# Performance work log

Measured on AMD Instinct MI355X. Metric: run time of the kernel, lower is better.

Reference implementation:

```python
import jax, jax.numpy as jnp
import numpy as np

T, B, D, H = 512, 64, 512, 512  # seq_len, batch, input_size, hidden_size


def setup_inputs() -> dict:
    key = jax.random.key(0)
    ks = jax.random.split(key, 7)
    s = jnp.float32(0.05)  # keep gates out of saturation
    return {
        "x": jax.random.normal(ks[0], (T, B, D), jnp.float32),
        "Wi_l0": jax.random.normal(ks[1], (2, 4 * H, D), jnp.float32) * s,
        "Wh_l0": jax.random.normal(ks[2], (2, 4 * H, H), jnp.float32) * s,
        "b_l0": jax.random.normal(ks[3], (2, 4 * H), jnp.float32) * s,
        "Wi_l1": jax.random.normal(ks[4], (2, 4 * H, 2 * H), jnp.float32) * s,
        "Wh_l1": jax.random.normal(ks[5], (2, 4 * H, H), jnp.float32) * s,
        "b_l1": jax.random.normal(ks[6], (2, 4 * H), jnp.float32) * s,
    }


def _lstm_dir(xs, Wi, Wh, b):
    """Run one LSTM direction over xs: [T, B, Din] -> ([T, B, H], h_T, c_T)."""
    Bsz = xs.shape[1]
    Hh = Wh.shape[-1]
    # Precompute input contribution for all timesteps (the big GEMM).
    gx = jnp.einsum('tbd,gd->tbg', xs, Wi) + b  # [T, B, 4H]

    def step(carry, gx_t):
        h, c = carry
        gates = gx_t + h @ Wh.T  # [B, 4H]
        i, f, g, o = jnp.split(gates, 4, axis=-1)
        c = jax.nn.sigmoid(f) * c + jax.nn.sigmoid(i) * jnp.tanh(g)
        h = jax.nn.sigmoid(o) * jnp.tanh(c)
        return (h, c), h

    h0 = jnp.zeros((Bsz, Hh), xs.dtype)
    (hT, cT), hs = jax.lax.scan(step, (h0, h0), gx)
    return hs, hT, cT


def _bilstm_layer(xs, Wi, Wh, b):
    hf, hTf, cTf = _lstm_dir(xs, Wi[0], Wh[0], b[0])
    hb, hTb, cTb = _lstm_dir(xs[::-1], Wi[1], Wh[1], b[1])
    # torch.stack(dim=2).view(T, B, -1) == concat along feature axis
    out = jnp.concatenate([hf, hb[::-1]], axis=-1)  # [T, B, 2H]
    return out, (hTf, hTb), (cTf, cTb)


def reference(x, Wi_l0, Wh_l0, b_l0, Wi_l1, Wh_l1, b_l1):
    o0, h0s, c0s = _bilstm_layer(x, Wi_l0, Wh_l0, b_l0)
    o1, h1s, c1s = _bilstm_layer(o0, Wi_l1, Wh_l1, b_l1)
    # state order: (layer0 fwd, layer0 bwd, layer1 fwd, layer1 bwd)
    h_n = jnp.stack(h0s + h1s, axis=0)  # [4, B, H]
    c_n = jnp.stack(c0s + c1s, axis=0)  # [4, B, H]
    return o1, (h_n, c_n)
```

## Files before the change

kernel.cpp:

```cpp
#include <hip/hip_runtime.h>
#include <stdint.h>


#define TT 512
#define BATCH 64
#define HH 512
#define NWG 64
#define NCOLS 32

typedef __attribute__((ext_vector_type(8))) short vshort8;
typedef __attribute__((ext_vector_type(4))) float vfloat4;
typedef __attribute__((ext_vector_type(4))) unsigned int vuint4;

__device__ __forceinline__ vfloat4 mfma16(vshort8 a, vshort8 b, vfloat4 c) {
    return __builtin_amdgcn_mfma_f32_16x16x32_bf16(a, b, c, 0, 0, 0);
}

__device__ __forceinline__ float sigmoidf_(float x) {
    return 1.f / (1.f + __expf(-x));
}
__device__ __forceinline__ float tanhf_(float x) {
    float e = __expf(2.f * x);
    return 1.f - 2.f / (e + 1.f);
}
__device__ __forceinline__ unsigned short f2bf(float f) {
    uint32_t u = __float_as_uint(f);
    uint32_t r = (u + 0x7fffu + ((u >> 16) & 1u)) >> 16;
    return (unsigned short)r;
}

__global__ void cvt_f32_bf16(const float* __restrict__ src,
                             unsigned short* __restrict__ dst, int n) {
    int i = (blockIdx.x * blockDim.x + threadIdx.x) * 4;
    if (i + 3 < n) {
        float4 v = *(const float4*)(src + i);
        uint2 p;
        p.x = (uint32_t)f2bf(v.x) | ((uint32_t)f2bf(v.y) << 16);
        p.y = (uint32_t)f2bf(v.z) | ((uint32_t)f2bf(v.w) << 16);
        *(uint2*)(dst + i) = p;
    }
}

template <int DIN, bool WRITE_BF16>
__launch_bounds__(256, 1)
__global__ void lstm_phase(const unsigned short* __restrict__ A,
                           const unsigned short* __restrict__ Wi,
                           const float* __restrict__ Whf,
                           const float* __restrict__ bias,
                           uint32_t* __restrict__ hbuf32,
                           unsigned short* __restrict__ obf,
                           float* __restrict__ of32,
                           float* __restrict__ hn,
                           float* __restrict__ cn)
{
    __shared__ unsigned short Wlds[NCOLS * DIN];
    __shared__ unsigned short Whlds[NCOLS * HH];

    const int tid = threadIdx.x;
    const int dir = blockIdx.x >> 6;
    const int wg = blockIdx.x & 63;
    const int j0 = wg * 8;
    const int lane = tid & 63;
    const int wave = tid >> 6;

    for (int chunk = tid; chunk < NCOLS * DIN / 8; chunk += 256) {
        int n = chunk / (DIN / 8);
        int k8 = (chunk % (DIN / 8)) * 8;
        int grow = (n >> 3) * HH + j0 + (n & 7);
        vshort8 v = *(const vshort8*)(Wi + ((size_t)dir * 4 * HH + grow) * DIN + k8);
        int byte = n * DIN * 2 + ((k8 * 2) ^ ((n & 7) << 4));
        *(vshort8*)((char*)Wlds + byte) = v;
    }
    for (int chunk = tid; chunk < NCOLS * HH / 8; chunk += 256) {
        int n = chunk / (HH / 8);
        int k8 = (chunk % (HH / 8)) * 8;
        int grow = (n >> 3) * HH + j0 + (n & 7);
        const float* src = Whf + ((size_t)dir * 4 * HH + grow) * HH + k8;
        float4 f0 = *(const float4*)(src);
        float4 f1 = *(const float4*)(src + 4);
        vshort8 v;
        v[0] = (short)f2bf(f0.x); v[1] = (short)f2bf(f0.y);
        v[2] = (short)f2bf(f0.z); v[3] = (short)f2bf(f0.w);
        v[4] = (short)f2bf(f1.x); v[5] = (short)f2bf(f1.y);
        v[6] = (short)f2bf(f1.z); v[7] = (short)f2bf(f1.w);
        int byte = n * HH * 2 + ((k8 * 2) ^ ((n & 7) << 4));
        *(vshort8*)((char*)Whlds + byte) = v;
    }
    __syncthreads();

    const int arow = wave * 16 + (lane & 15);
    const int kOff = (lane >> 4) * 8;
    const int klane = (lane >> 4) * 16;
    const int n0 = lane & 15;
    const int swz = (n0 & 7) << 4;
    const int nb0 = n0 * DIN * 2;
    const int nb1 = (16 + n0) * DIN * 2;
    const int nb0h = n0 * HH * 2;
    const int nb1h = (16 + n0) * HH * 2;
    const int grow0 = (n0 >> 3) * HH + j0 + (n0 & 7);
    const int grow1 = ((n0 >> 3) + 2) * HH + j0 + (n0 & 7);
    const float bias0 = bias[dir * 4 * HH + grow0];
    const float bias1 = bias[dir * 4 * HH + grow1];
    const bool lo = (lane & 8) == 0;
    const int jcol = j0 + (lane & 7);
    const int hrowb = wave * 16 + ((lane >> 4) << 2);
    const int scol = (lane & 15) * 32 + (lane >> 4) * 8;

    float cstate[4] = {0.f, 0.f, 0.f, 0.f};

    for (int s = 0; s < TT; ++s) {
        const int t = dir ? (TT - 1 - s) : s;

        vfloat4 acc0, acc1;
        acc0[0] = acc0[1] = acc0[2] = acc0[3] = bias0;
        acc1[0] = acc1[1] = acc1[2] = acc1[3] = bias1;

        const unsigned short* ap = A + ((size_t)t * BATCH + arow) * DIN + kOff;
#pragma unroll 8
        for (int kk = 0; kk < DIN / 32; ++kk) {
            vshort8 a = *(const vshort8*)(ap + kk * 32);
            int kb = kk * 64 + klane;
            vshort8 b0 = *(const vshort8*)((const char*)Wlds + nb0 + (kb ^ swz));
            vshort8 b1 = *(const vshort8*)((const char*)Wlds + nb1 + (kb ^ swz));
            acc0 = mfma16(a, b0, acc0);
            acc1 = mfma16(a, b1, acc1);
        }

        if (s > 0) {
            const uint32_t* rowbase =
                hbuf32 + (((dir << 1) | ((s - 1) & 1)) * BATCH + arow) * HH;
            const uint32_t* rbase = rowbase + kOff;
            const uint32_t want = (uint32_t)s;

            for (;;) {
                uint32_t sent;
                asm volatile(
                    "global_load_dword %0, %1, off sc0 sc1\n\t"
                    "s_waitcnt vmcnt(0)"
                    : "=v"(sent) : "v"(rowbase + scol) : "memory");
                if (!__any(((sent ^ want) & 0xffffu) != 0)) break;
                __builtin_amdgcn_s_sleep(1);
            }

            vuint4 hd[32];
            for (;;) {
#pragma unroll
                for (int q = 0; q < 32; ++q)
                    asm volatile("global_load_dwordx4 %0, %1, off sc0 sc1"
                                 : "=v"(hd[q])
                                 : "v"(rbase + (q >> 1) * 32 + (q & 1) * 4));
                asm volatile("s_waitcnt vmcnt(0)" ::: "memory");
                __builtin_amdgcn_sched_barrier(0);
                uint32_t diff = 0;
#pragma unroll
                for (int q = 0; q < 32; ++q)
                    diff |= (hd[q][0] ^ want) | (hd[q][1] ^ want) |
                            (hd[q][2] ^ want) | (hd[q][3] ^ want);
                if (!__any((diff & 0xffffu) != 0)) break;
                __builtin_amdgcn_s_sleep(1);
            }
            __builtin_amdgcn_sched_barrier(0);

#pragma unroll
            for (int kk = 0; kk < 16; ++kk) {
                uint32_t d0 = __builtin_amdgcn_perm(hd[2 * kk][1], hd[2 * kk][0], 0x07060302u);
                uint32_t d1 = __builtin_amdgcn_perm(hd[2 * kk][3], hd[2 * kk][2], 0x07060302u);
                uint32_t d2 = __builtin_amdgcn_perm(hd[2 * kk + 1][1], hd[2 * kk + 1][0], 0x07060302u);
                uint32_t d3 = __builtin_amdgcn_perm(hd[2 * kk + 1][3], hd[2 * kk + 1][2], 0x07060302u);
                vuint4 tt = {d0, d1, d2, d3};
                vshort8 ha = __builtin_bit_cast(vshort8, tt);
                int kb = kk * 64 + klane;
                vshort8 b0 = *(const vshort8*)((const char*)Whlds + nb0h + (kb ^ swz));
                vshort8 b1 = *(const vshort8*)((const char*)Whlds + nb1h + (kb ^ swz));
                acc0 = mfma16(ha, b0, acc0);
                acc1 = mfma16(ha, b1, acc1);
            }
        }

        float hval[4];
#pragma unroll
        for (int r = 0; r < 4; ++r) {
            float own0 = acc0[r], own1 = acc1[r];
            float oth0 = __shfl_xor(own0, 8, 64);
            float oth1 = __shfl_xor(own1, 8, 64);
            float iv = lo ? own0 : oth0;
            float fv = lo ? oth0 : own0;
            float gv = lo ? own1 : oth1;
            float ov = lo ? oth1 : own1;
            float cnew = sigmoidf_(fv) * cstate[r] + sigmoidf_(iv) * tanhf_(gv);
            cstate[r] = cnew;
            hval[r] = sigmoidf_(ov) * tanhf_(cnew);
        }

        uint32_t* hw = hbuf32 + (size_t)(((dir << 1) | (s & 1)) * BATCH) * HH;
        const int rA = lo ? 0 : 2;
        const uint32_t tagv = (uint32_t)(s + 1);
#pragma unroll
        for (int q = 0; q < 2; ++q) {
            int r = rA + q, row = hrowb + r;
            unsigned short hb = f2bf(hval[r]);
            uint32_t val = ((uint32_t)hb << 16) | tagv;
            uint32_t* wp = hw + row * HH + jcol;
            asm volatile("global_store_dword %0, %1, off sc0 sc1"
                         :: "v"(wp), "v"(val) : "memory");
            if constexpr (WRITE_BF16)
                obf[((size_t)t * BATCH + row) * (2 * HH) + dir * HH + jcol] = hb;
            else
                of32[((size_t)t * BATCH + row) * (2 * HH) + dir * HH + jcol] = hval[r];
        }
        if (s == TT - 1) {
#pragma unroll
            for (int q = 0; q < 2; ++q) {
                int r = rA + q, row = hrowb + r;
                hn[(dir * BATCH + row) * HH + jcol] = hval[r];
                cn[(dir * BATCH + row) * HH + jcol] = cstate[r];
            }
        }
    }
}

extern "C" void kernel_launch(void* const* d_in, const int* in_sizes, int n_in,
                              void* d_out, int out_size, void* d_ws, size_t ws_size,
                              hipStream_t stream) {
    const float* x = (const float*)d_in[0];
    const float* Wi0 = (const float*)d_in[1];
    const float* Wh0 = (const float*)d_in[2];
    const float* b0 = (const float*)d_in[3];
    const float* Wi1 = (const float*)d_in[4];
    const float* Wh1 = (const float*)d_in[5];
    const float* b1 = (const float*)d_in[6];

    char* ws = (char*)d_ws;
    uint32_t* hbufA = (uint32_t*)(ws);
    uint32_t* hbufB = (uint32_t*)(ws + 524288);
    unsigned short* wi0b = (unsigned short*)(ws + 1048576);
    unsigned short* wi1b = (unsigned short*)(ws + 5242880);
    unsigned short* xb = (unsigned short*)(ws + 13631488);
    unsigned short* o0 = (unsigned short*)(ws + 47185920);

    float* out = (float*)d_out;
    const size_t O1SZ = (size_t)TT * BATCH * 2 * HH;
    float* hn_base = out + O1SZ;
    float* cn_base = out + O1SZ + 4 * BATCH * HH;

    hipMemsetAsync(hbufA, 0, 1048576, stream);

    {
        int n;
        n = TT * BATCH * 512;
        cvt_f32_bf16<<<n / 1024, 256, 0, stream>>>(x, xb, n);
        n = 2 * 2048 * 512;
        cvt_f32_bf16<<<n / 1024, 256, 0, stream>>>(Wi0, wi0b, n);
        n = 2 * 2048 * 1024;
        cvt_f32_bf16<<<n / 1024, 256, 0, stream>>>(Wi1, wi1b, n);
    }

    lstm_phase<512, true><<<128, 256, 0, stream>>>(
        xb, wi0b, Wh0, b0, hbufA, o0, nullptr, hn_base, cn_base);

    lstm_phase<1024, false><<<128, 256, 0, stream>>>(
        o0, wi1b, Wh1, b1, hbufB, nullptr, out,
        hn_base + 2 * BATCH * HH, cn_base + 2 * BATCH * HH);
}
```

Before: 8.105 ms.

## Keep recurrent weights in registers and prefetch next step's input activations

Moves the recurrent weight slice from LDS into VGPRs for the whole sequence, removing per-step LDS reads in the critical h@Wh path. It also prefetches half of the next timestep's input activations during the current step and issues the sentinel poll before the input GEMM so its latency overlaps. The tag check is packed with perm ops, and the output stores move to inline asm after the h-buffer stores so the signal goes out first. This raises register pressure substantially (32 vshort8 for weights plus 16 for prefetch plus 32 for h data), which risks spills.

```diff
diff --git a/kernel.cpp b/kernel.cpp
--- a/kernel.cpp
+++ b/kernel.cpp
@@ -54,7 +54,6 @@
                            float* __restrict__ cn)
 {
     __shared__ unsigned short Wlds[NCOLS * DIN];
-    __shared__ unsigned short Whlds[NCOLS * HH];
 
     const int tid = threadIdx.x;
     const int dir = blockIdx.x >> 6;
@@ -71,21 +70,6 @@
         int byte = n * DIN * 2 + ((k8 * 2) ^ ((n & 7) << 4));
         *(vshort8*)((char*)Wlds + byte) = v;
     }
-    for (int chunk = tid; chunk < NCOLS * HH / 8; chunk += 256) {
-        int n = chunk / (HH / 8);
-        int k8 = (chunk % (HH / 8)) * 8;
-        int grow = (n >> 3) * HH + j0 + (n & 7);
-        const float* src = Whf + ((size_t)dir * 4 * HH + grow) * HH + k8;
-        float4 f0 = *(const float4*)(src);
-        float4 f1 = *(const float4*)(src + 4);
-        vshort8 v;
-        v[0] = (short)f2bf(f0.x); v[1] = (short)f2bf(f0.y);
-        v[2] = (short)f2bf(f0.z); v[3] = (short)f2bf(f0.w);
-        v[4] = (short)f2bf(f1.x); v[5] = (short)f2bf(f1.y);
-        v[6] = (short)f2bf(f1.z); v[7] = (short)f2bf(f1.w);
-        int byte = n * HH * 2 + ((k8 * 2) ^ ((n & 7) << 4));
-        *(vshort8*)((char*)Whlds + byte) = v;
-    }
     __syncthreads();
 
     const int arow = wave * 16 + (lane & 15);
@@ -95,8 +79,6 @@
     const int swz = (n0 & 7) << 4;
     const int nb0 = n0 * DIN * 2;
     const int nb1 = (16 + n0) * DIN * 2;
-    const int nb0h = n0 * HH * 2;
-    const int nb1h = (16 + n0) * HH * 2;
     const int grow0 = (n0 >> 3) * HH + j0 + (n0 & 7);
     const int grow1 = ((n0 >> 3) + 2) * HH + j0 + (n0 & 7);
     const float bias0 = bias[dir * 4 * HH + grow0];
@@ -106,19 +88,65 @@
     const int hrowb = wave * 16 + ((lane >> 4) << 2);
     const int scol = (lane & 15) * 32 + (lane >> 4) * 8;
 
+    const float* whf0 = Whf + ((size_t)dir * 4 * HH + grow0) * HH + kOff;
+    const float* whf1 = Whf + ((size_t)dir * 4 * HH + grow1) * HH + kOff;
+    vshort8 wh0r[16], wh1r[16];
+#pragma unroll
+    for (int kk = 0; kk < 16; ++kk) {
+        float4 a0 = *(const float4*)(whf0 + kk * 32);
+        float4 a1 = *(const float4*)(whf0 + kk * 32 + 4);
+        float4 b0 = *(const float4*)(whf1 + kk * 32);
+        float4 b1 = *(const float4*)(whf1 + kk * 32 + 4);
+        vshort8 a, b;
+        a[0] = (short)f2bf(a0.x); a[1] = (short)f2bf(a0.y);
+        a[2] = (short)f2bf(a0.z); a[3] = (short)f2bf(a0.w);
+        a[4] = (short)f2bf(a1.x); a[5] = (short)f2bf(a1.y);
+        a[6] = (short)f2bf(a1.z); a[7] = (short)f2bf(a1.w);
+        b[0] = (short)f2bf(b0.x); b[1] = (short)f2bf(b0.y);
+        b[2] = (short)f2bf(b0.z); b[3] = (short)f2bf(b0.w);
+        b[4] = (short)f2bf(b1.x); b[5] = (short)f2bf(b1.y);
+        b[6] = (short)f2bf(b1.z); b[7] = (short)f2bf(b1.w);
+        wh0r[kk] = a;
+        wh1r[kk] = b;
+        asm volatile("" : "+v"(wh0r[kk]), "+v"(wh1r[kk]));
+    }
+
     float cstate[4] = {0.f, 0.f, 0.f, 0.f};
+
+    vshort8 pre[16];
+    {
+        const int t0 = dir ? (TT - 1) : 0;
+        const unsigned short* ap0 = A + ((size_t)t0 * BATCH + arow) * DIN + kOff;
+#pragma unroll
+        for (int kk = 0; kk < 16; ++kk)
+            asm volatile("global_load_dwordx4 %0, %1, off"
+                         : "=v"(pre[kk]) : "v"(ap0 + kk * 32));
+    }
 
     for (int s = 0; s < TT; ++s) {
         const int t = dir ? (TT - 1 - s) : s;
+        const uint32_t want = (uint32_t)s;
+        const uint32_t* rowbase =
+            hbuf32 + (((dir << 1) | ((s - 1) & 1)) * BATCH + arow) * HH;
 
         vfloat4 acc0, acc1;
         acc0[0] = acc0[1] = acc0[2] = acc0[3] = bias0;
         acc1[0] = acc1[1] = acc1[2] = acc1[3] = bias1;
 
+        uint32_t sent;
+        if (s > 0) {
+            asm volatile("global_load_dword %0, %1, off sc0 sc1"
+                         : "=v"(sent) : "v"(rowbase + scol));
+            asm volatile("s_waitcnt vmcnt(5)" ::: "memory");
+        } else {
+            asm volatile("s_waitcnt vmcnt(0)" ::: "memory");
+        }
+        __builtin_amdgcn_sched_barrier(0);
+
         const unsigned short* ap = A + ((size_t)t * BATCH + arow) * DIN + kOff;
-#pragma unroll 8
+#pragma unroll
         for (int kk = 0; kk < DIN / 32; ++kk) {
-            vshort8 a = *(const vshort8*)(ap + kk * 32);
+            vshort8 a = (kk < 16) ? pre[kk] : *(const vshort8*)(ap + kk * 32);
             int kb = kk * 64 + klane;
             vshort8 b0 = *(const vshort8*)((const char*)Wlds + nb0 + (kb ^ swz));
             vshort8 b1 = *(const vshort8*)((const char*)Wlds + nb1 + (kb ^ swz));
@@ -126,23 +154,17 @@
             acc1 = mfma16(a, b1, acc1);
         }
 
+        vuint4 hd[32];
         if (s > 0) {
-            const uint32_t* rowbase =
-                hbuf32 + (((dir << 1) | ((s - 1) & 1)) * BATCH + arow) * HH;
+            for (;;) {
+                asm volatile("s_waitcnt vmcnt(0)" ::: "memory");
+                __builtin_amdgcn_sched_barrier(0);
+                if (!__any(((sent ^ want) & 0xffffu) != 0)) break;
+                asm volatile("global_load_dword %0, %1, off sc0 sc1"
+                             : "=v"(sent) : "v"(rowbase + scol));
+            }
             const uint32_t* rbase = rowbase + kOff;
-            const uint32_t want = (uint32_t)s;
-
-            for (;;) {
-                uint32_t sent;
-                asm volatile(
-                    "global_load_dword %0, %1, off sc0 sc1\n\t"
-                    "s_waitcnt vmcnt(0)"
-                    : "=v"(sent) : "v"(rowbase + scol) : "memory");
-                if (!__any(((sent ^ want) & 0xffffu) != 0)) break;
-                __builtin_amdgcn_s_sleep(1);
-            }
-
-            vuint4 hd[32];
+            const uint32_t want2 = want | (want << 16);
             for (;;) {
 #pragma unroll
                 for (int q = 0; q < 32; ++q)
@@ -153,14 +175,27 @@
                 __builtin_amdgcn_sched_barrier(0);
                 uint32_t diff = 0;
 #pragma unroll
-                for (int q = 0; q < 32; ++q)
-                    diff |= (hd[q][0] ^ want) | (hd[q][1] ^ want) |
-                            (hd[q][2] ^ want) | (hd[q][3] ^ want);
-                if (!__any((diff & 0xffffu) != 0)) break;
+                for (int q = 0; q < 32; ++q) {
+                    uint32_t t01 = __builtin_amdgcn_perm(hd[q][1], hd[q][0], 0x05040100u);
+                    uint32_t t23 = __builtin_amdgcn_perm(hd[q][3], hd[q][2], 0x05040100u);
+                    diff |= (t01 ^ want2) | (t23 ^ want2);
+                }
+                if (!__any(diff != 0)) break;
                 __builtin_amdgcn_s_sleep(1);
             }
             __builtin_amdgcn_sched_barrier(0);
-
+        }
+
+        if (s < TT - 1) {
+            const int tn = dir ? (TT - 2 - s) : (s + 1);
+            const unsigned short* apn = A + ((size_t)tn * BATCH + arow) * DIN + kOff;
+#pragma unroll
+            for (int kk = 0; kk < 16; ++kk)
+                asm volatile("global_load_dwordx4 %0, %1, off"
+                             : "=v"(pre[kk]) : "v"(apn + kk * 32));
+        }
+
+        if (s > 0) {
 #pragma unroll
             for (int kk = 0; kk < 16; ++kk) {
                 uint32_t d0 = __builtin_amdgcn_perm(hd[2 * kk][1], hd[2 * kk][0], 0x07060302u);
@@ -169,11 +204,8 @@
                 uint32_t d3 = __builtin_amdgcn_perm(hd[2 * kk + 1][3], hd[2 * kk + 1][2], 0x07060302u);
                 vuint4 tt = {d0, d1, d2, d3};
                 vshort8 ha = __builtin_bit_cast(vshort8, tt);
-                int kb = kk * 64 + klane;
-                vshort8 b0 = *(const vshort8*)((const char*)Whlds + nb0h + (kb ^ swz));
-                vshort8 b1 = *(const vshort8*)((const char*)Whlds + nb1h + (kb ^ swz));
-                acc0 = mfma16(ha, b0, acc0);
-                acc1 = mfma16(ha, b1, acc1);
+                acc0 = mfma16(ha, wh0r[kk], acc0);
+                acc1 = mfma16(ha, wh1r[kk], acc1);
             }
         }
 
@@ -195,18 +227,31 @@
         uint32_t* hw = hbuf32 + (size_t)(((dir << 1) | (s & 1)) * BATCH) * HH;
         const int rA = lo ? 0 : 2;
         const uint32_t tagv = (uint32_t)(s + 1);
+        unsigned short hb[2];
+        hb[0] = f2bf(hval[rA]);
+        hb[1] = f2bf(hval[rA + 1]);
 #pragma unroll
         for (int q = 0; q < 2; ++q) {
-            int r = rA + q, row = hrowb + r;
-            unsigned short hb = f2bf(hval[r]);
-            uint32_t val = ((uint32_t)hb << 16) | tagv;
+            int row = hrowb + rA + q;
+            uint32_t val = ((uint32_t)hb[q] << 16) | tagv;
             uint32_t* wp = hw + row * HH + jcol;
             asm volatile("global_store_dword %0, %1, off sc0 sc1"
                          :: "v"(wp), "v"(val) : "memory");
-            if constexpr (WRITE_BF16)
-                obf[((size_t)t * BATCH + row) * (2 * HH) + dir * HH + jcol] = hb;
-            else
-                of32[((size_t)t * BATCH + row) * (2 * HH) + dir * HH + jcol] = hval[r];
+        }
+#pragma unroll
+        for (int q = 0; q < 2; ++q) {
+            int row = hrowb + rA + q;
+            if constexpr (WRITE_BF16) {
+                unsigned short* op =
+                    obf + ((size_t)t * BATCH + row) * (2 * HH) + dir * HH + jcol;
+                uint32_t v32 = hb[q];
+                asm volatile("global_store_short %0, %1, off"
+                             :: "v"(op), "v"(v32) : "memory");
+            } else {
+                float* op = of32 + ((size_t)t * BATCH + row) * (2 * HH) + dir * HH + jcol;
+                asm volatile("global_store_dword %0, %1, off"
+                             :: "v"(op), "v"(hval[rA + q]) : "memory");
+            }
         }
         if (s == TT - 1) {
 #pragma unroll
```

Measured after the change: 10.29 ms. 27.0% more time.

## Replace tagged double-buffer polling with per-wave atomic counters and a ring buffer

Applied to the files above, without the earlier changes.

Each wave now waits on a per-wave arrival counter, which every workgroup atomically increments after storing its h slice, instead of spinning on tag bits spread through the hidden-state buffer. The hidden state goes into a 32-deep ring, so slots are reused rarely. The first read of the slot uses ordinary cached loads, and the uncached retry loop runs only if the tag check fails. The aim is to cut polling traffic and per-step sync latency on the sequential recurrence, at the cost of an atomic per wave per step, a vmcnt drain before it, and extra memsets for the larger ring buffers (ringB reuses the xb workspace).

```diff
diff --git a/kernel.cpp b/kernel.cpp
--- a/kernel.cpp
+++ b/kernel.cpp
@@ -5,8 +5,8 @@
 #define TT 512
 #define BATCH 64
 #define HH 512
-#define NWG 64
 #define NCOLS 32
+#define RING 32
 
 typedef __attribute__((ext_vector_type(8))) short vshort8;
 typedef __attribute__((ext_vector_type(4))) float vfloat4;
@@ -47,7 +47,8 @@
                            const unsigned short* __restrict__ Wi,
                            const float* __restrict__ Whf,
                            const float* __restrict__ bias,
-                           uint32_t* __restrict__ hbuf32,
+                           uint32_t* __restrict__ ring,
+                           uint32_t* __restrict__ cnt,
                            unsigned short* __restrict__ obf,
                            float* __restrict__ of32,
                            float* __restrict__ hn,
@@ -104,7 +105,7 @@
     const bool lo = (lane & 8) == 0;
     const int jcol = j0 + (lane & 7);
     const int hrowb = wave * 16 + ((lane >> 4) << 2);
-    const int scol = (lane & 15) * 32 + (lane >> 4) * 8;
+    uint32_t* const cpoll = cnt + (dir * 4 + wave) * 32;
 
     float cstate[4] = {0.f, 0.f, 0.f, 0.f};
 
@@ -127,39 +128,54 @@
         }
 
         if (s > 0) {
-            const uint32_t* rowbase =
-                hbuf32 + (((dir << 1) | ((s - 1) & 1)) * BATCH + arow) * HH;
-            const uint32_t* rbase = rowbase + kOff;
-            const uint32_t want = (uint32_t)s;
-
+            const uint32_t target = (uint32_t)(64 * s);
             for (;;) {
-                uint32_t sent;
+                uint32_t v;
                 asm volatile(
                     "global_load_dword %0, %1, off sc0 sc1\n\t"
                     "s_waitcnt vmcnt(0)"
-                    : "=v"(sent) : "v"(rowbase + scol) : "memory");
-                if (!__any(((sent ^ want) & 0xffffu) != 0)) break;
-                __builtin_amdgcn_s_sleep(1);
-            }
-
+                    : "=v"(v) : "v"(cpoll) : "memory");
+                if (__builtin_amdgcn_readfirstlane(v) >= target) break;
+            }
+            __builtin_amdgcn_sched_barrier(0);
+
+            const uint32_t* rbase =
+                ring + (((size_t)(dir * RING + ((s - 1) & (RING - 1)))) * BATCH + arow) * HH +
+                kOff;
             vuint4 hd[32];
-            for (;;) {
-#pragma unroll
-                for (int q = 0; q < 32; ++q)
-                    asm volatile("global_load_dwordx4 %0, %1, off sc0 sc1"
-                                 : "=v"(hd[q])
-                                 : "v"(rbase + (q >> 1) * 32 + (q & 1) * 4));
-                asm volatile("s_waitcnt vmcnt(0)" ::: "memory");
-                __builtin_amdgcn_sched_barrier(0);
-                uint32_t diff = 0;
-#pragma unroll
-                for (int q = 0; q < 32; ++q)
-                    diff |= (hd[q][0] ^ want) | (hd[q][1] ^ want) |
-                            (hd[q][2] ^ want) | (hd[q][3] ^ want);
-                if (!__any((diff & 0xffffu) != 0)) break;
-                __builtin_amdgcn_s_sleep(1);
-            }
-            __builtin_amdgcn_sched_barrier(0);
+#pragma unroll
+            for (int q = 0; q < 32; ++q)
+                hd[q] = *(const vuint4*)(rbase + (q >> 1) * 32 + (q & 1) * 4);
+
+            const uint32_t want = (uint32_t)s;
+            const uint32_t want2 = want | (want << 16);
+            uint32_t diff = 0;
+#pragma unroll
+            for (int q = 0; q < 32; ++q) {
+                uint32_t t01 = __builtin_amdgcn_perm(hd[q][1], hd[q][0], 0x05040100u);
+                uint32_t t23 = __builtin_amdgcn_perm(hd[q][3], hd[q][2], 0x05040100u);
+                diff |= (t01 ^ want2) | (t23 ^ want2);
+            }
+            if (__any(diff != 0)) {
+                for (;;) {
+#pragma unroll
+                    for (int q = 0; q < 32; ++q)
+                        asm volatile("global_load_dwordx4 %0, %1, off sc0 sc1"
+                                     : "=v"(hd[q])
+                                     : "v"(rbase + (q >> 1) * 32 + (q & 1) * 4));
+                    asm volatile("s_waitcnt vmcnt(0)" ::: "memory");
+                    __builtin_amdgcn_sched_barrier(0);
+                    uint32_t d2 = 0;
+#pragma unroll
+                    for (int q = 0; q < 32; ++q) {
+                        uint32_t t01 = __builtin_amdgcn_perm(hd[q][1], hd[q][0], 0x05040100u);
+                        uint32_t t23 = __builtin_amdgcn_perm(hd[q][3], hd[q][2], 0x05040100u);
+                        d2 |= (t01 ^ want2) | (t23 ^ want2);
+                    }
+                    if (!__any(d2 != 0)) break;
+                    __builtin_amdgcn_s_sleep(1);
+                }
+            }
 
 #pragma unroll
             for (int kk = 0; kk < 16; ++kk) {
@@ -192,7 +208,7 @@
             hval[r] = sigmoidf_(ov) * tanhf_(cnew);
         }
 
-        uint32_t* hw = hbuf32 + (size_t)(((dir << 1) | (s & 1)) * BATCH) * HH;
+        uint32_t* hw = ring + ((size_t)(dir * RING + (s & (RING - 1))) * BATCH) * HH;
         const int rA = lo ? 0 : 2;
         const uint32_t tagv = (uint32_t)(s + 1);
 #pragma unroll
@@ -216,6 +232,12 @@
                 cn[(dir * BATCH + row) * HH + jcol] = cstate[r];
             }
         }
+
+        if (s < TT - 1) {
+            asm volatile("s_waitcnt vmcnt(0)" ::: "memory");
+            __builtin_amdgcn_sched_barrier(0);
+            if (lane == 0) atomicAdd((unsigned int*)cpoll, 1u);
+        }
     }
 }
 
@@ -231,19 +253,22 @@
     const float* b1 = (const float*)d_in[6];
 
     char* ws = (char*)d_ws;
-    uint32_t* hbufA = (uint32_t*)(ws);
-    uint32_t* hbufB = (uint32_t*)(ws + 524288);
-    unsigned short* wi0b = (unsigned short*)(ws + 1048576);
-    unsigned short* wi1b = (unsigned short*)(ws + 5242880);
-    unsigned short* xb = (unsigned short*)(ws + 13631488);
-    unsigned short* o0 = (unsigned short*)(ws + 47185920);
+    uint32_t* cntA = (uint32_t*)(ws);
+    uint32_t* cntB = (uint32_t*)(ws + 2048);
+    uint32_t* ringA = (uint32_t*)(ws + 8192);
+    unsigned short* wi0b = (unsigned short*)(ws + 8396800);
+    unsigned short* wi1b = (unsigned short*)(ws + 12591104);
+    unsigned short* xb = (unsigned short*)(ws + 20979712);
+    uint32_t* ringB = (uint32_t*)(ws + 20979712);
+    unsigned short* o0 = (unsigned short*)(ws + 54534144);
 
     float* out = (float*)d_out;
     const size_t O1SZ = (size_t)TT * BATCH * 2 * HH;
     float* hn_base = out + O1SZ;
     float* cn_base = out + O1SZ + 4 * BATCH * HH;
 
-    hipMemsetAsync(hbufA, 0, 1048576, stream);
+    hipMemsetAsync(ws, 0, 4096, stream);
+    hipMemsetAsync(ringA, 0, 8388608, stream);
 
     {
         int n;
@@ -256,9 +281,11 @@
     }
 
     lstm_phase<512, true><<<128, 256, 0, stream>>>(
-        xb, wi0b, Wh0, b0, hbufA, o0, nullptr, hn_base, cn_base);
+        xb, wi0b, Wh0, b0, ringA, cntA, o0, nullptr, hn_base, cn_base);
+
+    hipMemsetAsync(ringB, 0, 8388608, stream);
 
     lstm_phase<1024, false><<<128, 256, 0, stream>>>(
-        o0, wi1b, Wh1, b1, hbufB, nullptr, out,
+        o0, wi1b, Wh1, b1, ringB, cntB, nullptr, out,
         hn_base + 2 * BATCH * HH, cn_base + 2 * BATCH * HH);
 }
```

Result: slower. 8.414 ms (+3.8%).
